# Kernel optimization log

Measured on AMD Instinct MI355X. Metric: run time of the kernel, lower is better.

The kernel has to match this reference:

```python
import jax, jax.numpy as jnp
import numpy as np
import math

B, M, C, H = 4, 2048, 512, 8
DQK = C // 4 // H  # 16 per-head query/key dim


def setup_inputs() -> dict:
    key = jax.random.key(0)
    ks = jax.random.split(key, 8)
    s = 0.02
    return {
        "x": jax.random.normal(ks[0], (B, M, C), dtype=jnp.float32),
        "mask": jax.random.randint(ks[1], (B, M), 0, 2, dtype=jnp.int32),
        "Wq": jax.random.normal(ks[2], (C, C // 4), dtype=jnp.float32) * s,
        "bq": jnp.zeros((C // 4,), dtype=jnp.float32),
        "Wk": jax.random.normal(ks[3], (C, C // 4), dtype=jnp.float32) * s,
        "bk": jnp.zeros((C // 4,), dtype=jnp.float32),
        "Wv": jax.random.normal(ks[4], (C, C), dtype=jnp.float32) * s,
        "bv": jnp.zeros((C,), dtype=jnp.float32),
        "gamma": jnp.ones((1,), dtype=jnp.float32),
    }


def reference(x, mask, Wq, bq, Wk, bk, Wv, bv, gamma):
    b, m, c = x.shape
    # projections, split heads: q/k -> (B, H, M, DQK), v -> (B, H, M, C//H)
    q = (x @ Wq + bq).reshape(b, m, H, -1).transpose(0, 2, 1, 3)
    k = (x @ Wk + bk).reshape(b, m, H, -1).transpose(0, 2, 1, 3)
    v = (x @ Wv + bv).reshape(b, m, H, -1).transpose(0, 2, 1, 3)
    scale = 1.0 / math.sqrt(q.shape[-1])
    scores = jnp.einsum('bhmd,bhnd->bhmn', q, k) * scale
    beta = jax.nn.softmax(jax.nn.relu(scores), axis=-1)  # act='relu' pre-softmax
    # att_drop = 0.0 -> identity
    mf = mask.astype(x.dtype)[:, None, None, :]  # (B,1,1,M)
    beta = beta * mf
    beta = beta / (beta.sum(-1, keepdims=True) + 1e-12)
    o = gamma * jnp.einsum('bhmn,bhnd->bhmd', beta, v)  # (B,H,M,C//H)
    return o.transpose(0, 2, 1, 3).reshape(b, m, c)
```

## Files before the change

### kernel.cpp

```cpp
#include <hip/hip_runtime.h>
#include <hip/hip_bf16.h>

#define MSEQ 2048

typedef __attribute__((ext_vector_type(8))) short short8;
typedef __attribute__((ext_vector_type(4))) float f32x4;

static __device__ __forceinline__ short bf16b(float f) {
    __hip_bfloat16 h = __float2bfloat16(f);
    return *reinterpret_cast<short*>(&h);
}

static __device__ __forceinline__ unsigned int pk2(float a, float b) {
    float2 f2; f2.x = a; f2.y = b;
    __hip_bfloat162 p = __float22bfloat162_rn(f2);
    return *reinterpret_cast<unsigned int*>(&p);
}

static __device__ __forceinline__ void gl_lds16(const void* g, void* l) {
    __builtin_amdgcn_global_load_lds(
        (const __attribute__((address_space(1))) unsigned int*)g,
        (__attribute__((address_space(3))) unsigned int*)l, 16, 0, 0);
}

__global__ __launch_bounds__(256) void wtrans_kernel(
    const float* __restrict__ Wq, const float* __restrict__ Wk,
    const float* __restrict__ Wv, unsigned short* __restrict__ WT)
{
    const int nt = blockIdx.x;
    const int kt = blockIdx.y;
    const int t  = threadIdx.x;
    const int k0 = kt*64;

    const float* W; int ld, n0;
    if (nt < 2)      { W = Wq; ld = 128; n0 = nt*64; }
    else if (nt < 4) { W = Wk; ld = 128; n0 = (nt-2)*64; }
    else             { W = Wv; ld = 512; n0 = (nt-4)*64; }

    __shared__ unsigned short Ts[64*72];

    #pragma unroll
    for (int s = 0; s < 4; ++s) {
        const int lin = s*256 + t;
        const int krow = lin >> 4, ng = lin & 15;
        const float4 v = *(const float4*)(W + (size_t)(k0+krow)*ld + n0 + ng*4);
        Ts[(ng*4+0)*72 + krow] = (unsigned short)bf16b(v.x);
        Ts[(ng*4+1)*72 + krow] = (unsigned short)bf16b(v.y);
        Ts[(ng*4+2)*72 + krow] = (unsigned short)bf16b(v.z);
        Ts[(ng*4+3)*72 + krow] = (unsigned short)bf16b(v.w);
    }
    __syncthreads();
    #pragma unroll
    for (int s = 0; s < 2; ++s) {
        const int lin = s*256 + t;
        const int nrow = lin >> 3, kg = lin & 7;
        *(short8*)(WT + (size_t)(nt*64 + nrow)*512 + k0 + kg*8) = *(const short8*)&Ts[nrow*72 + kg*8];
    }
}

__global__ __launch_bounds__(256, 4) void proj_mfma(
    const float* __restrict__ x, const unsigned short* __restrict__ WT,
    const float* __restrict__ bq, const float* __restrict__ bk, const float* __restrict__ bv,
    unsigned short* __restrict__ Qh, unsigned short* __restrict__ Kh, unsigned short* __restrict__ Vf)
{
    const int nt = blockIdx.x;
    const int r0 = blockIdx.y * 64;
    const int n0 = nt * 128;
    const int t = threadIdx.x, w = t >> 6, lane = t & 63, l15 = lane & 15, quad = lane >> 4;
    const int wqh = w >> 1, wch = w & 1;

    __shared__ short smem[128*72];
    short* As = smem;
    short* Bs = smem + 64*32;

    f32x4 acc[2][4];
    #pragma unroll
    for (int i = 0; i < 2; ++i)
        #pragma unroll
        for (int j = 0; j < 4; ++j) acc[i][j] = {0.f,0.f,0.f,0.f};

    const int brow = lane >> 2, bkg = lane & 3;

    for (int kk = 0; kk < 512; kk += 32) {
        #pragma unroll
        for (int s = 0; s < 2; ++s)
            gl_lds16(WT + (size_t)(n0 + w*32 + s*16 + brow)*512 + kk + bkg*8,
                     Bs + (w*32 + s*16)*32);
        #pragma unroll
        for (int s = 0; s < 2; ++s) {
            const int idx = s*256 + t;
            const int row = idx >> 3, cg = idx & 7;
            const float4 v = *(const float4*)(x + (size_t)(r0+row)*512 + kk + cg*4);
            uint2 uu; uu.x = pk2(v.x, v.y); uu.y = pk2(v.z, v.w);
            *(uint2*)&As[row*32 + cg*4] = uu;
        }
        __syncthreads();
        short8 Af[2], Bf[4];
        #pragma unroll
        for (int i = 0; i < 2; ++i) Af[i] = *(const short8*)&As[(wqh*32 + i*16 + l15)*32 + quad*8];
        #pragma unroll
        for (int j = 0; j < 4; ++j) Bf[j] = *(const short8*)&Bs[(wch*64 + j*16 + l15)*32 + quad*8];
        #pragma unroll
        for (int i = 0; i < 2; ++i)
            #pragma unroll
            for (int j = 0; j < 4; ++j)
                acc[i][j] = __builtin_amdgcn_mfma_f32_16x16x32_bf16(Af[i], Bf[j], acc[i][j], 0, 0, 0);
        __syncthreads();
    }

    const float* bias = (nt == 0) ? bq : (nt == 1) ? bk : (bv + (nt-2)*128);
    float bj[4];
    #pragma unroll
    for (int j = 0; j < 4; ++j) bj[j] = bias[wch*64 + j*16 + l15];

    const int b = r0 >> 11, key0 = r0 & 2047;
    if (nt < 2) {
        short* Ts = smem;
        #pragma unroll
        for (int i = 0; i < 2; ++i)
            #pragma unroll
            for (int j = 0; j < 4; ++j)
                #pragma unroll
                for (int r = 0; r < 4; ++r)
                    Ts[(wqh*32 + i*16 + quad*4 + r)*136 + wch*64 + j*16 + l15] =
                        bf16b(acc[i][j][r] + bj[j]);
        __syncthreads();
        unsigned short* Out = (nt == 0) ? Qh : Kh;
        #pragma unroll
        for (int s = 0; s < 4; ++s) {
            const int lin = s*256 + t, row = lin >> 4, seg = lin & 15;
            const int h = seg >> 1, dh = seg & 1;
            *(short8*)(Out + ((size_t)(b*8 + h)*MSEQ + key0 + row)*16 + dh*8) =
                *(const short8*)&Ts[row*136 + seg*8];
        }
    } else {
        short* Ts = smem;
        #pragma unroll
        for (int i = 0; i < 2; ++i)
            #pragma unroll
            for (int j = 0; j < 4; ++j)
                #pragma unroll
                for (int r = 0; r < 4; ++r)
                    Ts[(wch*64 + j*16 + l15)*72 + wqh*32 + i*16 + quad*4 + r] =
                        bf16b(acc[i][j][r] + bj[j]);
        __syncthreads();
        const int kt0 = key0 >> 6, h0 = (nt-2)*2;
        #pragma unroll
        for (int s = 0; s < 4; ++s) {
            const int lin = s*256 + t;
            const int lane_ = lin & 63, kh = (lin>>6)&1, ci = (lin>>7)&1;
            const int chh = (lin>>8)&1, h_l = (lin>>9)&1;
            const int l15_ = lane_ & 15, quad_ = lane_ >> 4;
            const int ch_local  = h_l*64 + (chh*2+ci)*16 + l15_;
            const int key_local = kh*32 + quad_*8;
            const size_t addr = (((((size_t)(b*8 + h0 + h_l)*32 + kt0)*2 + chh)*2 + ci)*2 + kh)*512
                                + lane_*8;
            *(short8*)(Vf + addr) = *(const short8*)&Ts[ch_local*72 + key_local];
        }
    }
}

__global__ __launch_bounds__(256, 4) void attn_mfma(
    const unsigned short* __restrict__ Qh, const unsigned short* __restrict__ Kh,
    const unsigned short* __restrict__ Vf, const int* __restrict__ mask,
    const float* __restrict__ gamma, float* __restrict__ out)
{
    const int m0 = blockIdx.x * 64;
    const int bh = blockIdx.y;
    const int b  = bh >> 3, h = bh & 7;
    const int t  = threadIdx.x;
    const int wave = t >> 6, lane = t & 63, l15 = lane & 15, quad = lane >> 4;
    const int qh = wave >> 1, chh = wave & 1;

    __shared__ short Ws[2*64*68];
    __shared__ float wsl[4*64];
    __shared__ float wsums[64];

    const short8 zz = {0,0,0,0,0,0,0,0};

    const unsigned short* Qrow = Qh + (size_t)(b*8 + h)*MSEQ*16;
    const unsigned short* Krow = Kh + (size_t)(b*8 + h)*MSEQ*16;
    const unsigned short* Vbh  = Vf + (size_t)(b*8 + h)*32*4096;
    const int* mrow = mask + b*MSEQ + wave*16 + quad*4;

    short8 qfrag[4];
    #pragma unroll
    for (int c = 0; c < 4; ++c)
        qfrag[c] = (quad < 2)
            ? *(const short8*)(Qrow + (size_t)(m0 + c*16 + l15)*16 + quad*8)
            : zz;

    f32x4 acc[2][2] = {{{0.f,0.f,0.f,0.f},{0.f,0.f,0.f,0.f}},
                       {{0.f,0.f,0.f,0.f},{0.f,0.f,0.f,0.f}}};
    float wsum_acc[4] = {0.f,0.f,0.f,0.f};

    short8 kfrag_n = (quad < 2)
        ? *(const short8*)(Krow + (size_t)(wave*16 + l15)*16 + quad*8) : zz;
    int4 mi_n = *(const int4*)(mrow);
    short8 Bfn[2][2];
    #pragma unroll
    for (int ci = 0; ci < 2; ++ci)
        #pragma unroll
        for (int kh = 0; kh < 2; ++kh)
            Bfn[ci][kh] = *(const short8*)(Vbh + (size_t)(((chh*2 + ci)*2 + kh))*512 + lane*8);

    for (int kt = 0; kt < 32; ++kt) {
        short* Wp = Ws + (kt & 1)*64*68;
        const short8 kfrag = kfrag_n;
        const int4 mi = mi_n;
        short8 Bf[2][2];
        #pragma unroll
        for (int ci = 0; ci < 2; ++ci)
            #pragma unroll
            for (int kh = 0; kh < 2; ++kh) Bf[ci][kh] = Bfn[ci][kh];

        if (kt < 31) {
            const int kn1 = (kt+1)*64;
            kfrag_n = (quad < 2)
                ? *(const short8*)(Krow + (size_t)(kn1 + wave*16 + l15)*16 + quad*8) : zz;
            mi_n = *(const int4*)(mrow + kn1);
            #pragma unroll
            for (int ci = 0; ci < 2; ++ci)
                #pragma unroll
                for (int kh = 0; kh < 2; ++kh)
                    Bfn[ci][kh] = *(const short8*)(Vbh
                        + (size_t)((((kt+1)*2 + chh)*2 + ci)*2 + kh)*512 + lane*8);
        }

        const float mk[4] = {(float)mi.x, (float)mi.y, (float)mi.z, (float)mi.w};

        #pragma unroll
        for (int c = 0; c < 4; ++c) {
            f32x4 s = {0.f,0.f,0.f,0.f};
            s = __builtin_amdgcn_mfma_f32_16x16x32_bf16(kfrag, qfrag[c], s, 0, 0, 0);
            float w0 = mk[0] * __expf(fmaxf(0.25f*s[0], 0.f));
            float w1 = mk[1] * __expf(fmaxf(0.25f*s[1], 0.f));
            float w2 = mk[2] * __expf(fmaxf(0.25f*s[2], 0.f));
            float w3 = mk[3] * __expf(fmaxf(0.25f*s[3], 0.f));
            uint2 uu; uu.x = pk2(w0, w1); uu.y = pk2(w2, w3);
            *(uint2*)&Wp[(c*16 + l15)*68 + wave*16 + quad*4] = uu;
            wsum_acc[c] += (w0 + w1) + (w2 + w3);
        }

        __syncthreads();

        short8 Af[2][2];
        #pragma unroll
        for (int si = 0; si < 2; ++si)
            #pragma unroll
            for (int kh = 0; kh < 2; ++kh)
                Af[si][kh] = *(const short8*)&Wp[((qh*2+si)*16 + l15)*68 + kh*32 + quad*8];
        #pragma unroll
        for (int si = 0; si < 2; ++si)
            #pragma unroll
            for (int ci = 0; ci < 2; ++ci)
                #pragma unroll
                for (int kh = 0; kh < 2; ++kh)
                    acc[si][ci] = __builtin_amdgcn_mfma_f32_16x16x32_bf16(
                        Af[si][kh], Bf[ci][kh], acc[si][ci], 0, 0, 0);
    }

    #pragma unroll
    for (int c = 0; c < 4; ++c) {
        float v = wsum_acc[c];
        v += __shfl_xor(v, 16, 64);
        v += __shfl_xor(v, 32, 64);
        if (quad == 0) wsl[wave*64 + c*16 + l15] = v;
    }
    __syncthreads();
    if (t < 64) wsums[t] = (wsl[t] + wsl[64+t]) + (wsl[128+t] + wsl[192+t]);
    __syncthreads();

    const float g = gamma[0];
    #pragma unroll
    for (int si = 0; si < 2; ++si) {
        #pragma unroll
        for (int r = 0; r < 4; ++r) {
            const int row = qh*32 + si*16 + quad*4 + r;
            const float inv = g / fmaxf(wsums[row], 1e-20f);
            #pragma unroll
            for (int ci = 0; ci < 2; ++ci) {
                const int col = chh*32 + ci*16 + l15;
                out[(size_t)(b*MSEQ + m0 + row)*512 + h*64 + col] = acc[si][ci][r] * inv;
            }
        }
    }
}

extern "C" void kernel_launch(void* const* d_in, const int* in_sizes, int n_in,
                              void* d_out, int out_size, void* d_ws, size_t ws_size,
                              hipStream_t stream) {
    const float* x     = (const float*)d_in[0];
    const int*   mask  = (const int*)  d_in[1];
    const float* Wq    = (const float*)d_in[2];
    const float* bq    = (const float*)d_in[3];
    const float* Wk    = (const float*)d_in[4];
    const float* bk    = (const float*)d_in[5];
    const float* Wv    = (const float*)d_in[6];
    const float* bv    = (const float*)d_in[7];
    const float* gamma = (const float*)d_in[8];
    float* outp = (float*)d_out;

    unsigned short* WT = (unsigned short*)d_ws;
    unsigned short* Qh = WT + (size_t)768*512;
    unsigned short* Kh = Qh + (size_t)8192*128;
    unsigned short* Vf = Kh + (size_t)8192*128;

    wtrans_kernel<<<dim3(12, 8), 256, 0, stream>>>(Wq, Wk, Wv, WT);
    proj_mfma<<<dim3(6, 128), 256, 0, stream>>>(x, WT, bq, bk, bv, Qh, Kh, Vf);
    attn_mfma<<<dim3(32, 32), 256, 0, stream>>>(Qh, Kh, Vf, mask, gamma, outp);
}
```

Before: 175.9 us.

## Warp-specialize attention into score-producer and PV-consumer waves

Doubles the attention block to 512 threads. Four waves compute QK scores, the exp weights and the row sums into the double-buffered LDS tile, while four other waves load V and run the PV MFMAs one tile behind, synchronised with a single barrier per iteration. Exp is also switched to exp2 with a folded log2e scale, and a select replaces the mask multiply. This is meant to overlap softmax ALU work with matrix work. In exchange it removes the register prefetch of V, adds an extra pipeline step, and may lower occupancy given the launch bound of 512 threads with 4 blocks.

After: 173.7 us. About the same (-1.3%).

```diff
diff --git a/kernel.cpp b/kernel.cpp
--- a/kernel.cpp
+++ b/kernel.cpp
@@ -160,7 +160,7 @@
     }
 }
 
-__global__ __launch_bounds__(256, 4) void attn_mfma(
+__global__ __launch_bounds__(512, 4) void attn_mfma(
     const unsigned short* __restrict__ Qh, const unsigned short* __restrict__ Kh,
     const unsigned short* __restrict__ Vf, const int* __restrict__ mask,
     const float* __restrict__ gamma, float* __restrict__ out)
@@ -170,118 +170,124 @@
     const int b  = bh >> 3, h = bh & 7;
     const int t  = threadIdx.x;
     const int wave = t >> 6, lane = t & 63, l15 = lane & 15, quad = lane >> 4;
-    const int qh = wave >> 1, chh = wave & 1;
 
     __shared__ short Ws[2*64*68];
     __shared__ float wsl[4*64];
     __shared__ float wsums[64];
 
     const short8 zz = {0,0,0,0,0,0,0,0};
-
-    const unsigned short* Qrow = Qh + (size_t)(b*8 + h)*MSEQ*16;
+    constexpr float SC = 0.25f * 1.44269504f;
+
+    short8 qfrag[4];
+    short8 kfrag_n = zz;
+    int4 mi_n = {0,0,0,0};
+    float wsum_acc[4] = {0.f,0.f,0.f,0.f};
     const unsigned short* Krow = Kh + (size_t)(b*8 + h)*MSEQ*16;
-    const unsigned short* Vbh  = Vf + (size_t)(b*8 + h)*32*4096;
     const int* mrow = mask + b*MSEQ + wave*16 + quad*4;
 
-    short8 qfrag[4];
-    #pragma unroll
-    for (int c = 0; c < 4; ++c)
-        qfrag[c] = (quad < 2)
-            ? *(const short8*)(Qrow + (size_t)(m0 + c*16 + l15)*16 + quad*8)
-            : zz;
-
+    const int w4 = wave & 3;
+    const int qh = w4 >> 1, chh = w4 & 1;
+    const unsigned short* Vbh = Vf + (size_t)(b*8 + h)*32*4096;
     f32x4 acc[2][2] = {{{0.f,0.f,0.f,0.f},{0.f,0.f,0.f,0.f}},
                        {{0.f,0.f,0.f,0.f},{0.f,0.f,0.f,0.f}}};
-    float wsum_acc[4] = {0.f,0.f,0.f,0.f};
-
-    short8 kfrag_n = (quad < 2)
-        ? *(const short8*)(Krow + (size_t)(wave*16 + l15)*16 + quad*8) : zz;
-    int4 mi_n = *(const int4*)(mrow);
-    short8 Bfn[2][2];
-    #pragma unroll
-    for (int ci = 0; ci < 2; ++ci)
-        #pragma unroll
-        for (int kh = 0; kh < 2; ++kh)
-            Bfn[ci][kh] = *(const short8*)(Vbh + (size_t)(((chh*2 + ci)*2 + kh))*512 + lane*8);
-
-    for (int kt = 0; kt < 32; ++kt) {
-        short* Wp = Ws + (kt & 1)*64*68;
-        const short8 kfrag = kfrag_n;
-        const int4 mi = mi_n;
-        short8 Bf[2][2];
-        #pragma unroll
-        for (int ci = 0; ci < 2; ++ci)
-            #pragma unroll
-            for (int kh = 0; kh < 2; ++kh) Bf[ci][kh] = Bfn[ci][kh];
-
-        if (kt < 31) {
-            const int kn1 = (kt+1)*64;
-            kfrag_n = (quad < 2)
-                ? *(const short8*)(Krow + (size_t)(kn1 + wave*16 + l15)*16 + quad*8) : zz;
-            mi_n = *(const int4*)(mrow + kn1);
-            #pragma unroll
-            for (int ci = 0; ci < 2; ++ci)
-                #pragma unroll
-                for (int kh = 0; kh < 2; ++kh)
-                    Bfn[ci][kh] = *(const short8*)(Vbh
-                        + (size_t)((((kt+1)*2 + chh)*2 + ci)*2 + kh)*512 + lane*8);
-        }
-
-        const float mk[4] = {(float)mi.x, (float)mi.y, (float)mi.z, (float)mi.w};
-
+
+    if (wave < 4) {
+        const unsigned short* Qrow = Qh + (size_t)(b*8 + h)*MSEQ*16;
+        #pragma unroll
+        for (int c = 0; c < 4; ++c)
+            qfrag[c] = (quad < 2)
+                ? *(const short8*)(Qrow + (size_t)(m0 + c*16 + l15)*16 + quad*8)
+                : zz;
+        kfrag_n = (quad < 2)
+            ? *(const short8*)(Krow + (size_t)(wave*16 + l15)*16 + quad*8) : zz;
+        mi_n = *(const int4*)(mrow);
+    }
+
+    for (int kt = 0; kt <= 32; ++kt) {
+        if (wave < 4) {
+            if (kt < 32) {
+                const short8 kfrag = kfrag_n;
+                const int4 mi = mi_n;
+                if (kt < 31) {
+                    kfrag_n = (quad < 2)
+                        ? *(const short8*)(Krow + (size_t)((kt+1)*64 + wave*16 + l15)*16 + quad*8)
+                        : zz;
+                    mi_n = *(const int4*)(mrow + (kt+1)*64);
+                }
+                short* Wp = Ws + (kt & 1)*64*68;
+                #pragma unroll
+                for (int c = 0; c < 4; ++c) {
+                    f32x4 s = {0.f,0.f,0.f,0.f};
+                    s = __builtin_amdgcn_mfma_f32_16x16x32_bf16(kfrag, qfrag[c], s, 0, 0, 0);
+                    const float e0 = __builtin_amdgcn_exp2f(fmaxf(SC*s[0], 0.f));
+                    const float e1 = __builtin_amdgcn_exp2f(fmaxf(SC*s[1], 0.f));
+                    const float e2 = __builtin_amdgcn_exp2f(fmaxf(SC*s[2], 0.f));
+                    const float e3 = __builtin_amdgcn_exp2f(fmaxf(SC*s[3], 0.f));
+                    const float w0 = mi.x ? e0 : 0.f;
+                    const float w1 = mi.y ? e1 : 0.f;
+                    const float w2 = mi.z ? e2 : 0.f;
+                    const float w3 = mi.w ? e3 : 0.f;
+                    uint2 uu; uu.x = pk2(w0, w1); uu.y = pk2(w2, w3);
+                    *(uint2*)&Wp[(c*16 + l15)*68 + wave*16 + quad*4] = uu;
+                    wsum_acc[c] += (w0 + w1) + (w2 + w3);
+                }
+            }
+        } else {
+            if (kt >= 1) {
+                const int j = kt - 1;
+                short8 Bf[2][2];
+                #pragma unroll
+                for (int ci = 0; ci < 2; ++ci)
+                    #pragma unroll
+                    for (int kh = 0; kh < 2; ++kh)
+                        Bf[ci][kh] = *(const short8*)(Vbh
+                            + (size_t)(((j*2 + chh)*2 + ci)*2 + kh)*512 + lane*8);
+                const short* Wp = Ws + (j & 1)*64*68;
+                short8 Af[2][2];
+                #pragma unroll
+                for (int si = 0; si < 2; ++si)
+                    #pragma unroll
+                    for (int kh = 0; kh < 2; ++kh)
+                        Af[si][kh] = *(const short8*)&Wp[((qh*2+si)*16 + l15)*68 + kh*32 + quad*8];
+                #pragma unroll
+                for (int si = 0; si < 2; ++si)
+                    #pragma unroll
+                    for (int ci = 0; ci < 2; ++ci)
+                        #pragma unroll
+                        for (int kh = 0; kh < 2; ++kh)
+                            acc[si][ci] = __builtin_amdgcn_mfma_f32_16x16x32_bf16(
+                                Af[si][kh], Bf[ci][kh], acc[si][ci], 0, 0, 0);
+            }
+        }
+        __syncthreads();
+    }
+
+    if (wave < 4) {
         #pragma unroll
         for (int c = 0; c < 4; ++c) {
-            f32x4 s = {0.f,0.f,0.f,0.f};
-            s = __builtin_amdgcn_mfma_f32_16x16x32_bf16(kfrag, qfrag[c], s, 0, 0, 0);
-            float w0 = mk[0] * __expf(fmaxf(0.25f*s[0], 0.f));
-            float w1 = mk[1] * __expf(fmaxf(0.25f*s[1], 0.f));
-            float w2 = mk[2] * __expf(fmaxf(0.25f*s[2], 0.f));
-            float w3 = mk[3] * __expf(fmaxf(0.25f*s[3], 0.f));
-            uint2 uu; uu.x = pk2(w0, w1); uu.y = pk2(w2, w3);
-            *(uint2*)&Wp[(c*16 + l15)*68 + wave*16 + quad*4] = uu;
-            wsum_acc[c] += (w0 + w1) + (w2 + w3);
-        }
-
-        __syncthreads();
-
-        short8 Af[2][2];
-        #pragma unroll
-        for (int si = 0; si < 2; ++si)
-            #pragma unroll
-            for (int kh = 0; kh < 2; ++kh)
-                Af[si][kh] = *(const short8*)&Wp[((qh*2+si)*16 + l15)*68 + kh*32 + quad*8];
-        #pragma unroll
-        for (int si = 0; si < 2; ++si)
-            #pragma unroll
-            for (int ci = 0; ci < 2; ++ci)
-                #pragma unroll
-                for (int kh = 0; kh < 2; ++kh)
-                    acc[si][ci] = __builtin_amdgcn_mfma_f32_16x16x32_bf16(
-                        Af[si][kh], Bf[ci][kh], acc[si][ci], 0, 0, 0);
-    }
-
-    #pragma unroll
-    for (int c = 0; c < 4; ++c) {
-        float v = wsum_acc[c];
-        v += __shfl_xor(v, 16, 64);
-        v += __shfl_xor(v, 32, 64);
-        if (quad == 0) wsl[wave*64 + c*16 + l15] = v;
+            float v = wsum_acc[c];
+            v += __shfl_xor(v, 16, 64);
+            v += __shfl_xor(v, 32, 64);
+            if (quad == 0) wsl[wave*64 + c*16 + l15] = v;
+        }
     }
     __syncthreads();
     if (t < 64) wsums[t] = (wsl[t] + wsl[64+t]) + (wsl[128+t] + wsl[192+t]);
     __syncthreads();
 
-    const float g = gamma[0];
-    #pragma unroll
-    for (int si = 0; si < 2; ++si) {
-        #pragma unroll
-        for (int r = 0; r < 4; ++r) {
-            const int row = qh*32 + si*16 + quad*4 + r;
-            const float inv = g / fmaxf(wsums[row], 1e-20f);
+    if (wave >= 4) {
+        const float g = gamma[0];
+        #pragma unroll
+        for (int si = 0; si < 2; ++si) {
             #pragma unroll
-            for (int ci = 0; ci < 2; ++ci) {
-                const int col = chh*32 + ci*16 + l15;
-                out[(size_t)(b*MSEQ + m0 + row)*512 + h*64 + col] = acc[si][ci][r] * inv;
+            for (int r = 0; r < 4; ++r) {
+                const int row = qh*32 + si*16 + quad*4 + r;
+                const float inv = g / fmaxf(wsums[row], 1e-20f);
+                #pragma unroll
+                for (int ci = 0; ci < 2; ++ci) {
+                    const int col = chh*32 + ci*16 + l15;
+                    out[(size_t)(b*MSEQ + m0 + row)*512 + h*64 + col] = acc[si][ci][r] * inv;
+                }
             }
         }
     }
@@ -308,5 +314,5 @@
 
     wtrans_kernel<<<dim3(12, 8), 256, 0, stream>>>(Wq, Wk, Wv, WT);
     proj_mfma<<<dim3(6, 128), 256, 0, stream>>>(x, WT, bq, bk, bv, Qh, Kh, Vf);
-    attn_mfma<<<dim3(32, 32), 256, 0, stream>>>(Qh, Kh, Vf, mask, gamma, outp);
-}
+    attn_mfma<<<dim3(32, 32), 512, 0, stream>>>(Qh, Kh, Vf, mask, gamma, outp);
+}
```
